# Performance work log

Measured on AMD Instinct MI355X. Metric: run time of the kernel, lower is better.

Reference implementation:

```python
import jax, jax.numpy as jnp
import numpy as np

N, NF1, NF2, NH, OUT, K = 16384, 2000, 10000, 512, 16, 19
BN_EPS = 1e-5

def _bn(x, g, b, m, v):
    # eval-mode BatchNorm1d with running stats
    return (x - m) * jax.lax.rsqrt(v + BN_EPS) * g + b


def setup_inputs() -> dict:
    key = jax.random.key(0)
    ks = jax.random.split(key, 24)
    f32 = jnp.float32
    def w(k, shape):
        return jax.random.normal(k, shape, f32) * 0.02
    inp = {
        "rna": jax.random.normal(ks[0], (N, NF1), f32),
        "atac": jax.random.normal(ks[1], (N, NF2), f32),
        "index_rna": jnp.arange(N, dtype=jnp.int32),
        "index_atac": jnp.arange(N, dtype=jnp.int32),
        "eps": jax.random.normal(ks[2], (N, OUT), f32),
        # RNA encoder
        "W_r1": w(ks[3], (NH, NF1)), "b_r1": jnp.zeros((NH,), f32),
        "g_r": jnp.ones((NH,), f32), "be_r": jnp.zeros((NH,), f32),
        "m_r": jnp.zeros((NH,), f32), "v_r": jnp.ones((NH,), f32),
        "W_rmu": w(ks[4], (OUT, NH)), "b_rmu": jnp.zeros((OUT,), f32),
        "W_rvar": w(ks[5], (OUT, NH)), "b_rvar": jnp.zeros((OUT,), f32),
        # ATAC encoder
        "W_a1": w(ks[6], (NH, NF2)), "b_a1": jnp.zeros((NH,), f32),
        "g_a": jnp.ones((NH,), f32), "be_a": jnp.zeros((NH,), f32),
        "m_a": jnp.zeros((NH,), f32), "v_a": jnp.ones((NH,), f32),
        "W_amu": w(ks[7], (OUT, NH)), "b_amu": jnp.zeros((OUT,), f32),
        "W_avar": w(ks[8], (OUT, NH)), "b_avar": jnp.zeros((OUT,), f32),
        # decoder
        "W_d1": w(ks[9], (NH, OUT)), "b_d1": jnp.zeros((NH,), f32),
        "g_d": jnp.ones((NH,), f32), "be_d": jnp.zeros((NH,), f32),
        "m_d": jnp.zeros((NH,), f32), "v_d": jnp.ones((NH,), f32),
        "W_d4": w(ks[10], (NF1 + NF2, NH)), "b_d4": jnp.zeros((NF1 + NF2,), f32),
        "cluster": jax.random.normal(ks[11], (K, OUT), f32),
    }
    return inp


def reference(rna, atac, index_rna, index_atac, eps,
              W_r1, b_r1, g_r, be_r, m_r, v_r, W_rmu, b_rmu, W_rvar, b_rvar,
              W_a1, b_a1, g_a, be_a, m_a, v_a, W_amu, b_amu, W_avar, b_avar,
              W_d1, b_d1, g_d, be_d, m_d, v_d, W_d4, b_d4, cluster):
    n = rna.shape[0]
    # encoders (dropout is identity in eval mode)
    h_rna = jax.nn.relu(_bn(rna @ W_r1.T + b_r1, g_r, be_r, m_r, v_r))
    zm_rna = h_rna @ W_rmu.T + b_rmu
    zv_rna = jnp.exp(h_rna @ W_rvar.T + b_rvar)
    h_atac = jax.nn.relu(_bn(atac @ W_a1.T + b_a1, g_a, be_a, m_a, v_a))
    zm_atac = h_atac @ W_amu.T + b_amu
    zv_atac = jnp.exp(h_atac @ W_avar.T + b_avar)
    # vectorized scatter replacing the per-sample Python loop
    mu = jnp.ones((n, 2, OUT), rna.dtype)
    var = jnp.ones((n, 2, OUT), rna.dtype)
    mask = jnp.zeros((n, 2, OUT), rna.dtype)
    mu = mu.at[index_rna, 0].set(zm_rna).at[index_atac, 1].set(zm_atac)
    var = var.at[index_rna, 0].set(zv_rna).at[index_atac, 1].set(zv_atac)
    mask = mask.at[index_rna, 0].set(1.0).at[index_atac, 1].set(1.0)
    # product of experts over the modality axis (axis=1)
    T = mask / var
    T_sum = T.sum(axis=1) + 1.0            # [n, OUT]
    z_mu = (mu * T).sum(axis=1) / T_sum
    z_var = 1.0 / T_sum
    # Normal(z_mu, scale=z_var).rsample() with externally supplied eps
    z = z_mu + z_var * eps
    # student-t style soft assignment to clusters
    d2 = jnp.sum((z[:, None, :] - cluster[None, :, :]) ** 2, axis=2)  # [n, K]
    q = 1.0 / (1.0 + d2)
    q = q / q.sum(axis=1, keepdims=True)
    # decoder
    h = jax.nn.relu(_bn(z @ W_d1.T + b_d1, g_d, be_d, m_d, v_d))
    recon_x = h @ W_d4.T + b_d4
    return (recon_x, z_mu, z_var, z, q)
```

## Files before the change

kernel.cpp:

```cpp
#include <hip/hip_runtime.h>

#define NS   16384
#define NF1c 2000
#define NF2c 10000
#define NH   512
#define KC   19
#define NREC 12000

typedef short bf16x8 __attribute__((ext_vector_type(8)));
typedef float f32x4  __attribute__((ext_vector_type(4)));

__device__ __forceinline__ unsigned short f2bf(float x) {
    unsigned int u = __builtin_bit_cast(unsigned int, x);
    u += 0x7FFFu + ((u >> 16) & 1u);
    return (unsigned short)(u >> 16);
}
__device__ __forceinline__ float bf2f(unsigned short h) {
    return __builtin_bit_cast(float, (unsigned int)h << 16);
}

__device__ __forceinline__ void sync_nodrain() {
    asm volatile("s_waitcnt lgkmcnt(0)" ::: "memory");
    __builtin_amdgcn_s_barrier();
    asm volatile("" ::: "memory");
}

__global__ void k_cvt(const float* __restrict__ s, unsigned short* __restrict__ d, int n4) {
    int i = blockIdx.x * blockDim.x + threadIdx.x;
    int st = gridDim.x * blockDim.x;
    for (; i < n4; i += st) {
        float4 f = ((const float4*)s)[i];
        ushort4 o;
        o.x = f2bf(f.x); o.y = f2bf(f.y); o.z = f2bf(f.z); o.w = f2bf(f.w);
        ((ushort4*)d)[i] = o;
    }
}

__global__ void k_prep_st(const float* __restrict__ g, const float* __restrict__ be,
                          const float* __restrict__ m, const float* __restrict__ v,
                          const float* __restrict__ b1,
                          float* __restrict__ s, float* __restrict__ t, int n) {
    int i = blockIdx.x * blockDim.x + threadIdx.x;
    if (i < n) {
        float sc = g[i] * rsqrtf(v[i] + 1e-5f);
        s[i] = sc;
        t[i] = be[i] + (b1[i] - m[i]) * sc;
    }
}

__global__ void k_zero(float* __restrict__ p, int n) {
    int i = blockIdx.x * blockDim.x + threadIdx.x;
    if (i < n) p[i] = 0.f;
}

template<int BK> __device__ __forceinline__ int swz(int r) {
    return (BK == 32) ? ((r >> 1) & 3) : (r & 7);
}

template<int EPI, int A_BF16, int BK>
__global__ __launch_bounds__(256)
void k_gemm(const void* __restrict__ Aptr, const unsigned short* __restrict__ B,
            int K, int Nn, int ntn,
            const float* __restrict__ sc, const float* __restrict__ sh,
            unsigned short* __restrict__ Hout, float* __restrict__ Fout)
{
    constexpr int CH = BK / 8;
    constexpr int JC = CH / 2;
    __shared__ __align__(16) unsigned short As[2][128 * BK];
    __shared__ __align__(16) unsigned short Bs[2][128 * BK];

    const int nwg = gridDim.x;
    const int q8  = nwg >> 3;
    const int L   = (blockIdx.x & 7) * q8 + (blockIdx.x >> 3);
    const int tn  = L % ntn, tm = L / ntn;

    const int tid  = threadIdx.x;
    const int wave = tid >> 6, lane = tid & 63;
    const int wr   = wave >> 1, wc = wave & 1;
    const int lo   = lane & 15, hi = lane >> 4;
    const int srow = tid >> 1, shalf = tid & 1;
    const long arow = (long)tm * 128 + srow;
    const int  brow = tn * 128 + srow;
    const bool bok  = (brow < Nn);

    const float*          Af  = (const float*)Aptr + arow * (long)K;
    const unsigned short* A16 = (const unsigned short*)Aptr + arow * (long)K;
    const unsigned short* Bp  = B + (long)brow * K;

    f32x4 acc[4][4];
#pragma unroll
    for (int i = 0; i < 4; i++)
#pragma unroll
        for (int j = 0; j < 4; j++) acc[i][j] = (f32x4){0.f, 0.f, 0.f, 0.f};

    float4 rfa[BK / 8];
    uint4  ra[JC];
    uint4  rb[JC];

    auto issue_load = [&](int k0, bool tail) {
        const int kb = k0 + shalf * (BK / 2);
        if (A_BF16) {
            if (!tail) {
#pragma unroll
                for (int j = 0; j < JC; j++) ra[j] = *(const uint4*)(A16 + kb + j * 8);
            } else {
#pragma unroll
                for (int j = 0; j < JC; j++) {
                    __align__(16) unsigned short t8[8];
#pragma unroll
                    for (int e = 0; e < 8; e++)
                        t8[e] = (kb + j * 8 + e < K) ? A16[kb + j * 8 + e] : (unsigned short)0;
                    ra[j] = *(uint4*)t8;
                }
            }
        } else {
            if (!tail) {
#pragma unroll
                for (int q = 0; q < BK / 8; q++) rfa[q] = *(const float4*)(Af + kb + q * 4);
            } else {
#pragma unroll
                for (int q = 0; q < BK / 8; q++) {
                    float4 f;
                    f.x = (kb + q * 4 + 0 < K) ? Af[kb + q * 4 + 0] : 0.f;
                    f.y = (kb + q * 4 + 1 < K) ? Af[kb + q * 4 + 1] : 0.f;
                    f.z = (kb + q * 4 + 2 < K) ? Af[kb + q * 4 + 2] : 0.f;
                    f.w = (kb + q * 4 + 3 < K) ? Af[kb + q * 4 + 3] : 0.f;
                    rfa[q] = f;
                }
            }
        }
#pragma unroll
        for (int j = 0; j < JC; j++) rb[j] = (uint4){0, 0, 0, 0};
        if (bok) {
            if (!tail) {
#pragma unroll
                for (int j = 0; j < JC; j++) rb[j] = *(const uint4*)(Bp + kb + j * 8);
            } else {
#pragma unroll
                for (int j = 0; j < JC; j++) {
                    __align__(16) unsigned short t8[8];
#pragma unroll
                    for (int e = 0; e < 8; e++)
                        t8[e] = (kb + j * 8 + e < K) ? Bp[kb + j * 8 + e] : (unsigned short)0;
                    rb[j] = *(uint4*)t8;
                }
            }
        }
    };

    auto write_lds = [&](int buf) {
        char* Ap = (char*)As[buf];
        char* Bq = (char*)Bs[buf];
        const int rbase = srow * (2 * BK);
        const int sw = swz<BK>(srow);
#pragma unroll
        for (int j = 0; j < JC; j++) {
            const int c = shalf * JC + j;
            const int pos = rbase + ((c ^ sw) << 4);
            uint4 av;
            if (A_BF16) {
                av = ra[j];
            } else {
                __align__(16) unsigned short u8[8];
#pragma unroll
                for (int e = 0; e < 8; e++) u8[e] = f2bf(((const float*)&rfa[2 * j])[e]);
                av = *(uint4*)u8;
            }
            *(uint4*)(Ap + pos) = av;
            *(uint4*)(Bq + pos) = rb[j];
        }
    };

    auto compute = [&](int buf) {
        const char* Ap = (const char*)As[buf];
        const char* Bq = (const char*)Bs[buf];
#pragma unroll
        for (int s = 0; s < BK / 32; s++) {
            bf16x8 af[4], bfv[4];
#pragma unroll
            for (int f = 0; f < 4; f++) {
                const int ar = wr * 64 + f * 16 + lo;
                af[f]  = *(const bf16x8*)(Ap + ar * (2 * BK) + (((s * 4 + hi) ^ swz<BK>(ar)) << 4));
                const int br = wc * 64 + f * 16 + lo;
                bfv[f] = *(const bf16x8*)(Bq + br * (2 * BK) + (((s * 4 + hi) ^ swz<BK>(br)) << 4));
            }
#pragma unroll
            for (int i = 0; i < 4; i++)
#pragma unroll
                for (int j = 0; j < 4; j++)
                    acc[i][j] = __builtin_amdgcn_mfma_f32_16x16x32_bf16(af[i], bfv[j], acc[i][j], 0, 0, 0);
        }
    };

    const int ntf = K / BK;
    const bool has_rem = (K % BK) != 0;
    const int nt = ntf + (has_rem ? 1 : 0);
    issue_load(0, has_rem && nt == 1);
    for (int t = 0; t < nt; ++t) {
        write_lds(t & 1);
        if (t + 1 < nt) issue_load((t + 1) * BK, has_rem && (t + 1 == nt - 1));
        sync_nodrain();
        compute(t & 1);
    }

#pragma unroll
    for (int i = 0; i < 4; i++) {
#pragma unroll
        for (int j = 0; j < 4; j++) {
            const int col = tn * 128 + wc * 64 + j * 16 + lo;
#pragma unroll
            for (int r = 0; r < 4; r++) {
                const long row = (long)tm * 128 + wr * 64 + i * 16 + hi * 4 + r;
                float v = acc[i][j][r];
                if (EPI == 0) {
                    v = fmaxf(v * sc[col] + sh[col], 0.f);
                    Hout[row * NH + col] = f2bf(v);
                } else {
                    if (col < Nn) Fout[row * (long)Nn + col] = v + sc[col];
                }
            }
        }
    }
}

__global__ __launch_bounds__(256)
void k_proj(const unsigned short* __restrict__ h_rna,
            const unsigned short* __restrict__ h_atac,
            const float* __restrict__ W_rmu, const float* __restrict__ b_rmu,
            const float* __restrict__ W_rvar, const float* __restrict__ b_rvar,
            const float* __restrict__ W_amu, const float* __restrict__ b_amu,
            const float* __restrict__ W_avar, const float* __restrict__ b_avar,
            const int* __restrict__ idx_rna, const int* __restrict__ idx_atac,
            float* __restrict__ mu0, float* __restrict__ var0,
            float* __restrict__ mu1, float* __restrict__ var1,
            float* __restrict__ mflag)
{
    __shared__ __align__(16) unsigned short hsh[4][2][NH];
    const int wave = threadIdx.x >> 6, lane = threadIdx.x & 63;
    const long i = (long)blockIdx.x * 4 + wave;
    *(uint4*)&hsh[wave][0][lane * 8] = *(const uint4*)(h_rna  + i * NH + lane * 8);
    *(uint4*)&hsh[wave][1][lane * 8] = *(const uint4*)(h_atac + i * NH + lane * 8);
    __syncthreads();
    const int mod = lane >> 5, oo = lane & 31;
    const int isv = oo >> 4, o = oo & 15;
    const float *W, *bias;
    if (mod == 0) { W = isv ? W_rvar : W_rmu; bias = isv ? b_rvar : b_rmu; }
    else          { W = isv ? W_avar : W_amu; bias = isv ? b_avar : b_amu; }
    const unsigned short* hr = hsh[wave][mod];
    const float* wrow = W + o * NH;
    float a = 0.f;
#pragma unroll 4
    for (int k = 0; k < NH; k += 4) {
        float4 w = *(const float4*)(wrow + k);
        a += bf2f(hr[k]) * w.x + bf2f(hr[k+1]) * w.y + bf2f(hr[k+2]) * w.z + bf2f(hr[k+3]) * w.w;
    }
    a += bias[o];
    const int tgt = (mod == 0) ? idx_rna[i] : idx_atac[i];
    float* mu  = mod ? mu1  : mu0;
    float* var = mod ? var1 : var0;
    if (!isv) mu[(long)tgt * 16 + o] = a;
    else      var[(long)tgt * 16 + o] = expf(a);
    if (oo == 0) mflag[(long)mod * NS + tgt] = 1.f;
}

__global__ __launch_bounds__(256)
void k_combine(const float* __restrict__ mu0, const float* __restrict__ var0,
               const float* __restrict__ mu1, const float* __restrict__ var1,
               const float* __restrict__ mflag,
               const float* __restrict__ eps, const float* __restrict__ cluster,
               const float* __restrict__ W_d1,
               const float* __restrict__ s_d, const float* __restrict__ t_d,
               float* __restrict__ o_zmu, float* __restrict__ o_zvar,
               float* __restrict__ o_z, float* __restrict__ o_q,
               unsigned short* __restrict__ h_d)
{
    __shared__ float zsh[4][16];
    const int wave = threadIdx.x >> 6, lane = threadIdx.x & 63;
    const long i = (long)blockIdx.x * 4 + wave;
    if (lane < 16) {
        const int d = lane;
        const float f0 = mflag[i], f1 = mflag[NS + i];
        float ts = 1.f, num = 0.f;
        if (f0 != 0.f) { float iv = 1.f / var0[i*16+d]; ts += iv; num += mu0[i*16+d] * iv; }
        if (f1 != 0.f) { float iv = 1.f / var1[i*16+d]; ts += iv; num += mu1[i*16+d] * iv; }
        const float zm = num / ts, zv = 1.f / ts;
        const float z = zm + zv * eps[i*16+d];
        o_zmu[i*16+d] = zm; o_zvar[i*16+d] = zv; o_z[i*16+d] = z;
        zsh[wave][d] = z;
    }
    __syncthreads();
    float zreg[16];
#pragma unroll
    for (int d = 0; d < 16; d++) zreg[d] = zsh[wave][d];
    float qk = 0.f;
    if (lane < KC) {
        float d2 = 0.f;
#pragma unroll
        for (int d = 0; d < 16; d++) { float df = zreg[d] - cluster[lane*16+d]; d2 += df*df; }
        qk = 1.f / (1.f + d2);
    }
    float ssum = qk;
#pragma unroll
    for (int off = 16; off > 0; off >>= 1) ssum += __shfl_xor(ssum, off, 32);
    if (lane < KC) o_q[i * KC + lane] = qk / ssum;
#pragma unroll
    for (int j = 0; j < 8; j++) {
        const int c = lane + 64 * j;
        float a = 0.f;
#pragma unroll
        for (int d = 0; d < 16; d += 4) {
            float4 w = *(const float4*)(W_d1 + c * 16 + d);
            a += zreg[d] * w.x + zreg[d+1] * w.y + zreg[d+2] * w.z + zreg[d+3] * w.w;
        }
        a = fmaxf(a * s_d[c] + t_d[c], 0.f);
        h_d[i * NH + c] = f2bf(a);
    }
}

extern "C" void kernel_launch(void* const* d_in, const int* in_sizes, int n_in,
                              void* d_out, int out_size, void* d_ws, size_t ws_size,
                              hipStream_t stream)
{
    const float* rna    = (const float*)d_in[0];
    const float* atac   = (const float*)d_in[1];
    const int*   i_rna  = (const int*)d_in[2];
    const int*   i_atac = (const int*)d_in[3];
    const float* eps    = (const float*)d_in[4];
    const float* W_r1   = (const float*)d_in[5];
    const float* b_r1   = (const float*)d_in[6];
    const float* g_r    = (const float*)d_in[7];
    const float* be_r   = (const float*)d_in[8];
    const float* m_r    = (const float*)d_in[9];
    const float* v_r    = (const float*)d_in[10];
    const float* W_rmu  = (const float*)d_in[11];
    const float* b_rmu  = (const float*)d_in[12];
    const float* W_rvar = (const float*)d_in[13];
    const float* b_rvar = (const float*)d_in[14];
    const float* W_a1   = (const float*)d_in[15];
    const float* b_a1   = (const float*)d_in[16];
    const float* g_a    = (const float*)d_in[17];
    const float* be_a   = (const float*)d_in[18];
    const float* m_a    = (const float*)d_in[19];
    const float* v_a    = (const float*)d_in[20];
    const float* W_amu  = (const float*)d_in[21];
    const float* b_amu  = (const float*)d_in[22];
    const float* W_avar = (const float*)d_in[23];
    const float* b_avar = (const float*)d_in[24];
    const float* W_d1   = (const float*)d_in[25];
    const float* b_d1   = (const float*)d_in[26];
    const float* g_d    = (const float*)d_in[27];
    const float* be_d   = (const float*)d_in[28];
    const float* m_d    = (const float*)d_in[29];
    const float* v_d    = (const float*)d_in[30];
    const float* W_d4   = (const float*)d_in[31];
    const float* b_d4   = (const float*)d_in[32];
    const float* clus   = (const float*)d_in[33];
    (void)in_sizes; (void)n_in; (void)out_size;

    char* w = (char*)d_ws;
    size_t off = 0;
    auto carve = [&](size_t bytes) { void* p = w + off; off += (bytes + 255) & ~(size_t)255; return p; };
    unsigned short* wr1b  = (unsigned short*)carve((size_t)NH * NF1c * 2);
    unsigned short* wa1b  = (unsigned short*)carve((size_t)NH * NF2c * 2);
    unsigned short* wd4b  = (unsigned short*)carve((size_t)NREC * NH * 2);
    unsigned short* hrna  = (unsigned short*)carve((size_t)NS * NH * 2);
    unsigned short* hatac = (unsigned short*)carve((size_t)NS * NH * 2);
    unsigned short* hd    = (unsigned short*)carve((size_t)NS * NH * 2);
    float* mu0   = (float*)carve((size_t)NS * 16 * 4);
    float* var0  = (float*)carve((size_t)NS * 16 * 4);
    float* mu1   = (float*)carve((size_t)NS * 16 * 4);
    float* var1  = (float*)carve((size_t)NS * 16 * 4);
    float* mflag = (float*)carve((size_t)2 * NS * 4);
    float* st    = (float*)carve((size_t)6 * NH * 4);
    if (off > ws_size) return;

    float* s_r = st;          float* t_r = st + NH;
    float* s_a = st + 2*NH;   float* t_a = st + 3*NH;
    float* s_d = st + 4*NH;   float* t_d = st + 5*NH;

    float* out    = (float*)d_out;
    float* o_rec  = out;
    float* o_zmu  = out + (size_t)NS * NREC;
    float* o_zvar = o_zmu + (size_t)NS * 16;
    float* o_z    = o_zvar + (size_t)NS * 16;
    float* o_q    = o_z + (size_t)NS * 16;

    k_cvt<<<1024, 256, 0, stream>>>(W_r1, wr1b, NH * NF1c / 4);
    k_cvt<<<2048, 256, 0, stream>>>(W_a1, wa1b, NH * NF2c / 4);
    k_cvt<<<2048, 256, 0, stream>>>(W_d4, wd4b, NREC * NH / 4);
    k_prep_st<<<2, 256, 0, stream>>>(g_r, be_r, m_r, v_r, b_r1, s_r, t_r, NH);
    k_prep_st<<<2, 256, 0, stream>>>(g_a, be_a, m_a, v_a, b_a1, s_a, t_a, NH);
    k_prep_st<<<2, 256, 0, stream>>>(g_d, be_d, m_d, v_d, b_d1, s_d, t_d, NH);
    k_zero<<<(2 * NS + 255) / 256, 256, 0, stream>>>(mflag, 2 * NS);

    dim3 blk(256);
    k_gemm<0, 0, 64><<<512, blk, 0, stream>>>(rna,  wr1b, NF1c, NH, 4, s_r, t_r, hrna,  nullptr);
    k_gemm<0, 0, 64><<<512, blk, 0, stream>>>(atac, wa1b, NF2c, NH, 4, s_a, t_a, hatac, nullptr);
    k_proj<<<NS / 4, blk, 0, stream>>>(hrna, hatac, W_rmu, b_rmu, W_rvar, b_rvar,
                                       W_amu, b_amu, W_avar, b_avar, i_rna, i_atac,
                                       mu0, var0, mu1, var1, mflag);
    k_combine<<<NS / 4, blk, 0, stream>>>(mu0, var0, mu1, var1, mflag, eps, clus,
                                          W_d1, s_d, t_d, o_zmu, o_zvar, o_z, o_q, hd);
    k_gemm<1, 1, 32><<<94 * 128, blk, 0, stream>>>(hd, wd4b, NH, NREC, 94, b_d4, nullptr, nullptr, o_rec);
}
```

Measured before the change: 1.227 ms.

## Deepen GEMM global-load prefetch to two register stages with occupancy hint

The GEMM main loop now keeps two register staging buffers, so global loads for tile t+2 are issued while tile t is written to LDS and computed. This hides more global-memory latency. The loop is unrolled by two, with a tail for odd tile counts. The kernel also gets a launch_bounds minimum of 2 blocks per CU, and float-to-bf16 conversion now uses the hip_bfloat16 constructor with packed 32-bit writes. The extra staging registers may raise register pressure, which conflicts with the two-block occupancy target and could cause spills.

After: 1.294 ms. 5.5% more time.

```diff
diff --git a/kernel.cpp b/kernel.cpp
--- a/kernel.cpp
+++ b/kernel.cpp
@@ -1,4 +1,5 @@
 #include <hip/hip_runtime.h>
+#include <hip/hip_bf16.h>
 
 #define NS   16384
 #define NF1c 2000
@@ -11,9 +12,7 @@
 typedef float f32x4  __attribute__((ext_vector_type(4)));
 
 __device__ __forceinline__ unsigned short f2bf(float x) {
-    unsigned int u = __builtin_bit_cast(unsigned int, x);
-    u += 0x7FFFu + ((u >> 16) & 1u);
-    return (unsigned short)(u >> 16);
+    return __builtin_bit_cast(unsigned short, __hip_bfloat16(x));
 }
 __device__ __forceinline__ float bf2f(unsigned short h) {
     return __builtin_bit_cast(float, (unsigned int)h << 16);
@@ -58,14 +57,13 @@
 }
 
 template<int EPI, int A_BF16, int BK>
-__global__ __launch_bounds__(256)
+__global__ __launch_bounds__(256, 2)
 void k_gemm(const void* __restrict__ Aptr, const unsigned short* __restrict__ B,
             int K, int Nn, int ntn,
             const float* __restrict__ sc, const float* __restrict__ sh,
             unsigned short* __restrict__ Hout, float* __restrict__ Fout)
 {
-    constexpr int CH = BK / 8;
-    constexpr int JC = CH / 2;
+    constexpr int JC = BK / 16;
     __shared__ __align__(16) unsigned short As[2][128 * BK];
     __shared__ __align__(16) unsigned short Bs[2][128 * BK];
 
@@ -93,16 +91,19 @@
 #pragma unroll
         for (int j = 0; j < 4; j++) acc[i][j] = (f32x4){0.f, 0.f, 0.f, 0.f};
 
-    float4 rfa[BK / 8];
-    uint4  ra[JC];
-    uint4  rb[JC];
-
-    auto issue_load = [&](int k0, bool tail) {
+    struct Stage {
+        float4 af[BK / 8];
+        uint4  ah[JC];
+        uint4  b[JC];
+    };
+    Stage s0, s1;
+
+    auto issue = [&](Stage& S, int k0, bool tail) {
         const int kb = k0 + shalf * (BK / 2);
         if (A_BF16) {
             if (!tail) {
 #pragma unroll
-                for (int j = 0; j < JC; j++) ra[j] = *(const uint4*)(A16 + kb + j * 8);
+                for (int j = 0; j < JC; j++) S.ah[j] = *(const uint4*)(A16 + kb + j * 8);
             } else {
 #pragma unroll
                 for (int j = 0; j < JC; j++) {
@@ -110,13 +111,13 @@
 #pragma unroll
                     for (int e = 0; e < 8; e++)
                         t8[e] = (kb + j * 8 + e < K) ? A16[kb + j * 8 + e] : (unsigned short)0;
-                    ra[j] = *(uint4*)t8;
+                    S.ah[j] = *(uint4*)t8;
                 }
             }
         } else {
             if (!tail) {
 #pragma unroll
-                for (int q = 0; q < BK / 8; q++) rfa[q] = *(const float4*)(Af + kb + q * 4);
+                for (int q = 0; q < BK / 8; q++) S.af[q] = *(const float4*)(Af + kb + q * 4);
             } else {
 #pragma unroll
                 for (int q = 0; q < BK / 8; q++) {
@@ -125,16 +126,16 @@
                     f.y = (kb + q * 4 + 1 < K) ? Af[kb + q * 4 + 1] : 0.f;
                     f.z = (kb + q * 4 + 2 < K) ? Af[kb + q * 4 + 2] : 0.f;
                     f.w = (kb + q * 4 + 3 < K) ? Af[kb + q * 4 + 3] : 0.f;
-                    rfa[q] = f;
+                    S.af[q] = f;
                 }
             }
         }
 #pragma unroll
-        for (int j = 0; j < JC; j++) rb[j] = (uint4){0, 0, 0, 0};
+        for (int j = 0; j < JC; j++) S.b[j] = (uint4){0, 0, 0, 0};
         if (bok) {
             if (!tail) {
 #pragma unroll
-                for (int j = 0; j < JC; j++) rb[j] = *(const uint4*)(Bp + kb + j * 8);
+                for (int j = 0; j < JC; j++) S.b[j] = *(const uint4*)(Bp + kb + j * 8);
             } else {
 #pragma unroll
                 for (int j = 0; j < JC; j++) {
@@ -142,13 +143,13 @@
 #pragma unroll
                     for (int e = 0; e < 8; e++)
                         t8[e] = (kb + j * 8 + e < K) ? Bp[kb + j * 8 + e] : (unsigned short)0;
-                    rb[j] = *(uint4*)t8;
+                    S.b[j] = *(uint4*)t8;
                 }
             }
         }
     };
 
-    auto write_lds = [&](int buf) {
+    auto write = [&](int buf, Stage& S) {
         char* Ap = (char*)As[buf];
         char* Bq = (char*)Bs[buf];
         const int rbase = srow * (2 * BK);
@@ -159,19 +160,23 @@
             const int pos = rbase + ((c ^ sw) << 4);
             uint4 av;
             if (A_BF16) {
-                av = ra[j];
+                av = S.ah[j];
             } else {
-                __align__(16) unsigned short u8[8];
-#pragma unroll
-                for (int e = 0; e < 8; e++) u8[e] = f2bf(((const float*)&rfa[2 * j])[e]);
-                av = *(uint4*)u8;
+                unsigned int* w32 = (unsigned int*)&av;
+#pragma unroll
+                for (int e = 0; e < 4; e++) {
+                    const float* fp = (const float*)&S.af[2 * j];
+                    unsigned int lo16 = f2bf(fp[2 * e]);
+                    unsigned int hi16 = f2bf(fp[2 * e + 1]);
+                    w32[e] = lo16 | (hi16 << 16);
+                }
             }
             *(uint4*)(Ap + pos) = av;
-            *(uint4*)(Bq + pos) = rb[j];
+            *(uint4*)(Bq + pos) = S.b[j];
         }
     };
 
-    auto compute = [&](int buf) {
+    auto comp = [&](int buf) {
         const char* Ap = (const char*)As[buf];
         const char* Bq = (const char*)Bs[buf];
 #pragma unroll
@@ -193,14 +198,26 @@
     };
 
     const int ntf = K / BK;
-    const bool has_rem = (K % BK) != 0;
-    const int nt = ntf + (has_rem ? 1 : 0);
-    issue_load(0, has_rem && nt == 1);
-    for (int t = 0; t < nt; ++t) {
-        write_lds(t & 1);
-        if (t + 1 < nt) issue_load((t + 1) * BK, has_rem && (t + 1 == nt - 1));
+    const bool rem = (K % BK) != 0;
+    const int nt = ntf + (rem ? 1 : 0);
+
+    issue(s0, 0, rem && nt == 1);
+    if (nt > 1) issue(s1, BK, rem && nt == 2);
+    int t = 0;
+    for (; t + 2 <= nt; t += 2) {
+        write(0, s0);
+        if (t + 2 < nt) issue(s0, (t + 2) * BK, rem && (t + 2 == nt - 1));
         sync_nodrain();
-        compute(t & 1);
+        comp(0);
+        write(1, s1);
+        if (t + 3 < nt) issue(s1, (t + 3) * BK, rem && (t + 3 == nt - 1));
+        sync_nodrain();
+        comp(1);
+    }
+    if (t < nt) {
+        write(0, s0);
+        sync_nodrain();
+        comp(0);
     }
 
 #pragma unroll
```

## Retile encoder GEMMs to 128x64 tiles with BK=32 and raise occupancy

Applied to the files above, without the earlier changes.

The GEMM template now fixes BK at 32 and takes the N tile width as a parameter. The encoder GEMMs use 128x64 tiles over twice as many workgroups, and launch bounds request 4 waves per SIMD. MFMA issue is wrapped in s_setprio, and float-to-bf16 conversion switches to the HIP intrinsic with packed writes. The aim is more resident workgroups, so the streaming fp32 activation loads get better latency hiding. In exchange, B tiles are re-read across more workgroups and each LDS stage carries a smaller K slice.

Result: slower. 1.751 ms (+42.8%).

```diff
diff --git a/kernel.cpp b/kernel.cpp
--- a/kernel.cpp
+++ b/kernel.cpp
@@ -1,4 +1,5 @@
 #include <hip/hip_runtime.h>
+#include <hip/hip_bf16.h>
 
 #define NS   16384
 #define NF1c 2000
@@ -11,9 +12,7 @@
 typedef float f32x4  __attribute__((ext_vector_type(4)));
 
 __device__ __forceinline__ unsigned short f2bf(float x) {
-    unsigned int u = __builtin_bit_cast(unsigned int, x);
-    u += 0x7FFFu + ((u >> 16) & 1u);
-    return (unsigned short)(u >> 16);
+    return __builtin_bit_cast(unsigned short, __hip_bfloat16(x));
 }
 __device__ __forceinline__ float bf2f(unsigned short h) {
     return __builtin_bit_cast(float, (unsigned int)h << 16);
@@ -53,21 +52,18 @@
     if (i < n) p[i] = 0.f;
 }
 
-template<int BK> __device__ __forceinline__ int swz(int r) {
-    return (BK == 32) ? ((r >> 1) & 3) : (r & 7);
-}
-
-template<int EPI, int A_BF16, int BK>
-__global__ __launch_bounds__(256)
+__device__ __forceinline__ int swz(int r) { return (r >> 1) & 3; }
+
+template<int EPI, int A_BF16, int BN>
+__global__ __launch_bounds__(256, 4)
 void k_gemm(const void* __restrict__ Aptr, const unsigned short* __restrict__ B,
             int K, int Nn, int ntn,
             const float* __restrict__ sc, const float* __restrict__ sh,
             unsigned short* __restrict__ Hout, float* __restrict__ Fout)
 {
-    constexpr int CH = BK / 8;
-    constexpr int JC = CH / 2;
-    __shared__ __align__(16) unsigned short As[2][128 * BK];
-    __shared__ __align__(16) unsigned short Bs[2][128 * BK];
+    constexpr int NB = BN / 32;
+    __shared__ __align__(16) unsigned short As[2][128 * 32];
+    __shared__ __align__(16) unsigned short Bs[2][BN * 32];
 
     const int nwg = gridDim.x;
     const int q8  = nwg >> 3;
@@ -78,136 +74,154 @@
     const int wave = tid >> 6, lane = tid & 63;
     const int wr   = wave >> 1, wc = wave & 1;
     const int lo   = lane & 15, hi = lane >> 4;
-    const int srow = tid >> 1, shalf = tid & 1;
-    const long arow = (long)tm * 128 + srow;
-    const int  brow = tn * 128 + srow;
+
+    const int srowA = tid >> 1, shalfA = tid & 1;
+    const int srowB  = (BN == 128) ? (tid >> 1) : (tid >> 2);
+    const int schB   = (BN == 128) ? ((tid & 1) * 2) : (tid & 3);
+    constexpr int BCH = (BN == 128) ? 2 : 1;
+
+    const long arow = (long)tm * 128 + srowA;
+    const int  brow = tn * BN + srowB;
     const bool bok  = (brow < Nn);
 
     const float*          Af  = (const float*)Aptr + arow * (long)K;
     const unsigned short* A16 = (const unsigned short*)Aptr + arow * (long)K;
     const unsigned short* Bp  = B + (long)brow * K;
 
-    f32x4 acc[4][4];
+    f32x4 acc[4][NB];
 #pragma unroll
     for (int i = 0; i < 4; i++)
 #pragma unroll
-        for (int j = 0; j < 4; j++) acc[i][j] = (f32x4){0.f, 0.f, 0.f, 0.f};
-
-    float4 rfa[BK / 8];
-    uint4  ra[JC];
-    uint4  rb[JC];
-
-    auto issue_load = [&](int k0, bool tail) {
-        const int kb = k0 + shalf * (BK / 2);
+        for (int j = 0; j < NB; j++) acc[i][j] = (f32x4){0.f, 0.f, 0.f, 0.f};
+
+    float4 rfa[4];
+    uint4  rah[2];
+    uint4  rb[BCH];
+
+    auto issue = [&](int k0, bool tail) {
+        const int kbA = k0 + shalfA * 16;
         if (A_BF16) {
             if (!tail) {
 #pragma unroll
-                for (int j = 0; j < JC; j++) ra[j] = *(const uint4*)(A16 + kb + j * 8);
+                for (int j = 0; j < 2; j++) rah[j] = *(const uint4*)(A16 + kbA + j * 8);
             } else {
 #pragma unroll
-                for (int j = 0; j < JC; j++) {
+                for (int j = 0; j < 2; j++) {
                     __align__(16) unsigned short t8[8];
 #pragma unroll
                     for (int e = 0; e < 8; e++)
-                        t8[e] = (kb + j * 8 + e < K) ? A16[kb + j * 8 + e] : (unsigned short)0;
-                    ra[j] = *(uint4*)t8;
+                        t8[e] = (kbA + j * 8 + e < K) ? A16[kbA + j * 8 + e] : (unsigned short)0;
+                    rah[j] = *(uint4*)t8;
                 }
             }
         } else {
             if (!tail) {
 #pragma unroll
-                for (int q = 0; q < BK / 8; q++) rfa[q] = *(const float4*)(Af + kb + q * 4);
+                for (int q = 0; q < 4; q++) rfa[q] = *(const float4*)(Af + kbA + q * 4);
             } else {
 #pragma unroll
-                for (int q = 0; q < BK / 8; q++) {
+                for (int q = 0; q < 4; q++) {
                     float4 f;
-                    f.x = (kb + q * 4 + 0 < K) ? Af[kb + q * 4 + 0] : 0.f;
-                    f.y = (kb + q * 4 + 1 < K) ? Af[kb + q * 4 + 1] : 0.f;
-                    f.z = (kb + q * 4 + 2 < K) ? Af[kb + q * 4 + 2] : 0.f;
-                    f.w = (kb + q * 4 + 3 < K) ? Af[kb + q * 4 + 3] : 0.f;
+                    f.x = (kbA + q * 4 + 0 < K) ? Af[kbA + q * 4 + 0] : 0.f;
+                    f.y = (kbA + q * 4 + 1 < K) ? Af[kbA + q * 4 + 1] : 0.f;
+                    f.z = (kbA + q * 4 + 2 < K) ? Af[kbA + q * 4 + 2] : 0.f;
+                    f.w = (kbA + q * 4 + 3 < K) ? Af[kbA + q * 4 + 3] : 0.f;
                     rfa[q] = f;
                 }
             }
         }
 #pragma unroll
-        for (int j = 0; j < JC; j++) rb[j] = (uint4){0, 0, 0, 0};
+        for (int j = 0; j < BCH; j++) rb[j] = (uint4){0, 0, 0, 0};
         if (bok) {
             if (!tail) {
 #pragma unroll
-                for (int j = 0; j < JC; j++) rb[j] = *(const uint4*)(Bp + kb + j * 8);
+                for (int j = 0; j < BCH; j++)
+                    rb[j] = *(const uint4*)(Bp + k0 + (schB + j) * 8);
             } else {
 #pragma unroll
-                for (int j = 0; j < JC; j++) {
+                for (int j = 0; j < BCH; j++) {
                     __align__(16) unsigned short t8[8];
 #pragma unroll
-                    for (int e = 0; e < 8; e++)
-                        t8[e] = (kb + j * 8 + e < K) ? Bp[kb + j * 8 + e] : (unsigned short)0;
+                    for (int e = 0; e < 8; e++) {
+                        const int kk = k0 + (schB + j) * 8 + e;
+                        t8[e] = (kk < K) ? Bp[kk] : (unsigned short)0;
+                    }
                     rb[j] = *(uint4*)t8;
                 }
             }
         }
     };
 
-    auto write_lds = [&](int buf) {
+    auto write = [&](int buf) {
         char* Ap = (char*)As[buf];
         char* Bq = (char*)Bs[buf];
-        const int rbase = srow * (2 * BK);
-        const int sw = swz<BK>(srow);
-#pragma unroll
-        for (int j = 0; j < JC; j++) {
-            const int c = shalf * JC + j;
-            const int pos = rbase + ((c ^ sw) << 4);
+        const int rbaseA = srowA * 64;
+        const int swA = swz(srowA);
+#pragma unroll
+        for (int j = 0; j < 2; j++) {
+            const int c = shalfA * 2 + j;
             uint4 av;
             if (A_BF16) {
-                av = ra[j];
+                av = rah[j];
             } else {
-                __align__(16) unsigned short u8[8];
-#pragma unroll
-                for (int e = 0; e < 8; e++) u8[e] = f2bf(((const float*)&rfa[2 * j])[e]);
-                av = *(uint4*)u8;
+                unsigned int* w32 = (unsigned int*)&av;
+                const float* fp = (const float*)&rfa[2 * j];
+#pragma unroll
+                for (int e = 0; e < 4; e++) {
+                    unsigned int l16 = f2bf(fp[2 * e]);
+                    unsigned int h16 = f2bf(fp[2 * e + 1]);
+                    w32[e] = l16 | (h16 << 16);
+                }
             }
-            *(uint4*)(Ap + pos) = av;
-            *(uint4*)(Bq + pos) = rb[j];
-        }
+            *(uint4*)(Ap + rbaseA + ((c ^ swA) << 4)) = av;
+        }
+        const int rbaseB = srowB * 64;
+        const int swB = swz(srowB);
+#pragma unroll
+        for (int j = 0; j < BCH; j++)
+            *(uint4*)(Bq + rbaseB + (((schB + j) ^ swB) << 4)) = rb[j];
     };
 
-    auto compute = [&](int buf) {
+    auto comp = [&](int buf) {
         const char* Ap = (const char*)As[buf];
         const char* Bq = (const char*)Bs[buf];
-#pragma unroll
-        for (int s = 0; s < BK / 32; s++) {
-            bf16x8 af[4], bfv[4];
-#pragma unroll
-            for (int f = 0; f < 4; f++) {
-                const int ar = wr * 64 + f * 16 + lo;
-                af[f]  = *(const bf16x8*)(Ap + ar * (2 * BK) + (((s * 4 + hi) ^ swz<BK>(ar)) << 4));
-                const int br = wc * 64 + f * 16 + lo;
-                bfv[f] = *(const bf16x8*)(Bq + br * (2 * BK) + (((s * 4 + hi) ^ swz<BK>(br)) << 4));
-            }
-#pragma unroll
-            for (int i = 0; i < 4; i++)
-#pragma unroll
-                for (int j = 0; j < 4; j++)
-                    acc[i][j] = __builtin_amdgcn_mfma_f32_16x16x32_bf16(af[i], bfv[j], acc[i][j], 0, 0, 0);
-        }
+        bf16x8 af[4], bfv[NB];
+#pragma unroll
+        for (int f = 0; f < 4; f++) {
+            const int ar = wr * 64 + f * 16 + lo;
+            af[f] = *(const bf16x8*)(Ap + ar * 64 + ((hi ^ swz(ar)) << 4));
+        }
+#pragma unroll
+        for (int f = 0; f < NB; f++) {
+            const int br = wc * (BN / 2) + f * 16 + lo;
+            bfv[f] = *(const bf16x8*)(Bq + br * 64 + ((hi ^ swz(br)) << 4));
+        }
+        __builtin_amdgcn_s_setprio(1);
+#pragma unroll
+        for (int i = 0; i < 4; i++)
+#pragma unroll
+            for (int j = 0; j < NB; j++)
+                acc[i][j] = __builtin_amdgcn_mfma_f32_16x16x32_bf16(af[i], bfv[j], acc[i][j], 0, 0, 0);
+        __builtin_amdgcn_s_setprio(0);
     };
 
-    const int ntf = K / BK;
-    const bool has_rem = (K % BK) != 0;
-    const int nt = ntf + (has_rem ? 1 : 0);
-    issue_load(0, has_rem && nt == 1);
+    const int ntf = K / 32;
+    const bool rem = (K % 32) != 0;
+    const int nt = ntf + (rem ? 1 : 0);
+
+    issue(0, rem && nt == 1);
     for (int t = 0; t < nt; ++t) {
-        write_lds(t & 1);
-        if (t + 1 < nt) issue_load((t + 1) * BK, has_rem && (t + 1 == nt - 1));
+        write(t & 1);
+        if (t + 1 < nt) issue((t + 1) * 32, rem && (t + 1 == nt - 1));
         sync_nodrain();
-        compute(t & 1);
+        comp(t & 1);
     }
 
 #pragma unroll
     for (int i = 0; i < 4; i++) {
 #pragma unroll
-        for (int j = 0; j < 4; j++) {
-            const int col = tn * 128 + wc * 64 + j * 16 + lo;
+        for (int j = 0; j < NB; j++) {
+            const int col = tn * BN + wc * (BN / 2) + j * 16 + lo;
 #pragma unroll
             for (int r = 0; r < 4; r++) {
                 const long row = (long)tm * 128 + wr * 64 + i * 16 + hi * 4 + r;
@@ -394,12 +408,12 @@
     k_zero<<<(2 * NS + 255) / 256, 256, 0, stream>>>(mflag, 2 * NS);
 
     dim3 blk(256);
-    k_gemm<0, 0, 64><<<512, blk, 0, stream>>>(rna,  wr1b, NF1c, NH, 4, s_r, t_r, hrna,  nullptr);
-    k_gemm<0, 0, 64><<<512, blk, 0, stream>>>(atac, wa1b, NF2c, NH, 4, s_a, t_a, hatac, nullptr);
+    k_gemm<0, 0, 64><<<1024, blk, 0, stream>>>(rna,  wr1b, NF1c, NH, 8, s_r, t_r, hrna,  nullptr);
+    k_gemm<0, 0, 64><<<1024, blk, 0, stream>>>(atac, wa1b, NF2c, NH, 8, s_a, t_a, hatac, nullptr);
     k_proj<<<NS / 4, blk, 0, stream>>>(hrna, hatac, W_rmu, b_rmu, W_rvar, b_rvar,
                                        W_amu, b_amu, W_avar, b_avar, i_rna, i_atac,
                                        mu0, var0, mu1, var1, mflag);
     k_combine<<<NS / 4, blk, 0, stream>>>(mu0, var0, mu1, var1, mflag, eps, clus,
                                           W_d1, s_d, t_d, o_zmu, o_zvar, o_z, o_q, hd);
-    k_gemm<1, 1, 32><<<94 * 128, blk, 0, stream>>>(hd, wd4b, NH, NREC, 94, b_d4, nullptr, nullptr, o_rec);
-}
+    k_gemm<1, 1, 128><<<94 * 128, blk, 0, stream>>>(hd, wd4b, NH, NREC, 94, b_d4, nullptr, nullptr, o_rec);
+}
```

## Add dedicated decoder GEMM using direct global-to-LDS loads with padded weights

Applied to the files above, without the earlier changes.

Replaces the templated bf16 decoder GEMM with a dedicated kernel that loads tiles straight from global memory into LDS via global_load_lds, using a pre-swizzled source address. W_d4 is converted into a zero-padded buffer so that no bounds checks are needed on B loads. MFMA blocks run under raised s_setprio. The change also swaps the manual f32-to-bf16 rounding for the HIP bfloat16 conversion and packs pairs into 32-bit words. The decoder GEMM writes about 786MB of fp32 output, so the store path probably still dominates and the load-path gains may be small.

Result: no change. 1.225 ms (-0.2%).

```diff
diff --git a/kernel.cpp b/kernel.cpp
--- a/kernel.cpp
+++ b/kernel.cpp
@@ -1,19 +1,19 @@
 #include <hip/hip_runtime.h>
-
-#define NS   16384
-#define NF1c 2000
-#define NF2c 10000
-#define NH   512
-#define KC   19
-#define NREC 12000
+#include <hip/hip_bf16.h>
+
+#define NS    16384
+#define NF1c  2000
+#define NF2c  10000
+#define NH    512
+#define KC    19
+#define NREC  12000
+#define NRECP 12032
 
 typedef short bf16x8 __attribute__((ext_vector_type(8)));
 typedef float f32x4  __attribute__((ext_vector_type(4)));
 
 __device__ __forceinline__ unsigned short f2bf(float x) {
-    unsigned int u = __builtin_bit_cast(unsigned int, x);
-    u += 0x7FFFu + ((u >> 16) & 1u);
-    return (unsigned short)(u >> 16);
+    return __builtin_bit_cast(unsigned short, __hip_bfloat16(x));
 }
 __device__ __forceinline__ float bf2f(unsigned short h) {
     return __builtin_bit_cast(float, (unsigned int)h << 16);
@@ -23,6 +23,16 @@
     asm volatile("s_waitcnt lgkmcnt(0)" ::: "memory");
     __builtin_amdgcn_s_barrier();
     asm volatile("" ::: "memory");
+}
+
+template<int BK> __device__ __forceinline__ int swz(int r) {
+    return (BK == 32) ? ((r >> 1) & 3) : (r & 7);
+}
+
+__device__ __forceinline__ void gload16(const unsigned short* g, unsigned short* l) {
+    __builtin_amdgcn_global_load_lds(
+        (const __attribute__((address_space(1))) void*)g,
+        (__attribute__((address_space(3))) void*)l, 16, 0, 0);
 }
 
 __global__ void k_cvt(const float* __restrict__ s, unsigned short* __restrict__ d, int n4) {
@@ -33,6 +43,26 @@
         ushort4 o;
         o.x = f2bf(f.x); o.y = f2bf(f.y); o.z = f2bf(f.z); o.w = f2bf(f.w);
         ((ushort4*)d)[i] = o;
+    }
+}
+
+__global__ void k_cvt_pad(const float* __restrict__ s, unsigned short* __restrict__ d,
+                          int K, int Rv, long nchunks) {
+    long i = (long)blockIdx.x * blockDim.x + threadIdx.x;
+    const long stp = (long)gridDim.x * blockDim.x;
+    const int Kp8 = K / 8;
+    for (; i < nchunks; i += stp) {
+        const long row = i / Kp8;
+        const int  col = (int)(i - row * Kp8) * 8;
+        __align__(16) unsigned short u[8] = {0, 0, 0, 0, 0, 0, 0, 0};
+        if (row < Rv) {
+            const float* p = s + row * (long)K + col;
+            float4 f0 = *(const float4*)p;
+            float4 f1 = *(const float4*)(p + 4);
+            u[0] = f2bf(f0.x); u[1] = f2bf(f0.y); u[2] = f2bf(f0.z); u[3] = f2bf(f0.w);
+            u[4] = f2bf(f1.x); u[5] = f2bf(f1.y); u[6] = f2bf(f1.z); u[7] = f2bf(f1.w);
+        }
+        *(uint4*)(d + row * (long)K + col) = *(uint4*)u;
     }
 }
 
@@ -53,19 +83,14 @@
     if (i < n) p[i] = 0.f;
 }
 
-template<int BK> __device__ __forceinline__ int swz(int r) {
-    return (BK == 32) ? ((r >> 1) & 3) : (r & 7);
-}
-
-template<int EPI, int A_BF16, int BK>
 __global__ __launch_bounds__(256)
 void k_gemm(const void* __restrict__ Aptr, const unsigned short* __restrict__ B,
             int K, int Nn, int ntn,
             const float* __restrict__ sc, const float* __restrict__ sh,
-            unsigned short* __restrict__ Hout, float* __restrict__ Fout)
+            unsigned short* __restrict__ Hout)
 {
-    constexpr int CH = BK / 8;
-    constexpr int JC = CH / 2;
+    constexpr int BK = 64;
+    constexpr int JC = BK / 16;
     __shared__ __align__(16) unsigned short As[2][128 * BK];
     __shared__ __align__(16) unsigned short Bs[2][128 * BK];
 
@@ -83,9 +108,8 @@
     const int  brow = tn * 128 + srow;
     const bool bok  = (brow < Nn);
 
-    const float*          Af  = (const float*)Aptr + arow * (long)K;
-    const unsigned short* A16 = (const unsigned short*)Aptr + arow * (long)K;
-    const unsigned short* Bp  = B + (long)brow * K;
+    const float*          Af = (const float*)Aptr + arow * (long)K;
+    const unsigned short* Bp = B + (long)brow * K;
 
     f32x4 acc[4][4];
 #pragma unroll
@@ -94,39 +118,22 @@
         for (int j = 0; j < 4; j++) acc[i][j] = (f32x4){0.f, 0.f, 0.f, 0.f};
 
     float4 rfa[BK / 8];
-    uint4  ra[JC];
     uint4  rb[JC];
 
-    auto issue_load = [&](int k0, bool tail) {
+    auto issue = [&](int k0, bool tail) {
         const int kb = k0 + shalf * (BK / 2);
-        if (A_BF16) {
-            if (!tail) {
-#pragma unroll
-                for (int j = 0; j < JC; j++) ra[j] = *(const uint4*)(A16 + kb + j * 8);
-            } else {
-#pragma unroll
-                for (int j = 0; j < JC; j++) {
-                    __align__(16) unsigned short t8[8];
-#pragma unroll
-                    for (int e = 0; e < 8; e++)
-                        t8[e] = (kb + j * 8 + e < K) ? A16[kb + j * 8 + e] : (unsigned short)0;
-                    ra[j] = *(uint4*)t8;
-                }
-            }
+        if (!tail) {
+#pragma unroll
+            for (int q = 0; q < BK / 8; q++) rfa[q] = *(const float4*)(Af + kb + q * 4);
         } else {
-            if (!tail) {
-#pragma unroll
-                for (int q = 0; q < BK / 8; q++) rfa[q] = *(const float4*)(Af + kb + q * 4);
-            } else {
-#pragma unroll
-                for (int q = 0; q < BK / 8; q++) {
-                    float4 f;
-                    f.x = (kb + q * 4 + 0 < K) ? Af[kb + q * 4 + 0] : 0.f;
-                    f.y = (kb + q * 4 + 1 < K) ? Af[kb + q * 4 + 1] : 0.f;
-                    f.z = (kb + q * 4 + 2 < K) ? Af[kb + q * 4 + 2] : 0.f;
-                    f.w = (kb + q * 4 + 3 < K) ? Af[kb + q * 4 + 3] : 0.f;
-                    rfa[q] = f;
-                }
+#pragma unroll
+            for (int q = 0; q < BK / 8; q++) {
+                float4 f;
+                f.x = (kb + q * 4 + 0 < K) ? Af[kb + q * 4 + 0] : 0.f;
+                f.y = (kb + q * 4 + 1 < K) ? Af[kb + q * 4 + 1] : 0.f;
+                f.z = (kb + q * 4 + 2 < K) ? Af[kb + q * 4 + 2] : 0.f;
+                f.w = (kb + q * 4 + 3 < K) ? Af[kb + q * 4 + 3] : 0.f;
+                rfa[q] = f;
             }
         }
 #pragma unroll
@@ -148,7 +155,7 @@
         }
     };
 
-    auto write_lds = [&](int buf) {
+    auto write = [&](int buf) {
         char* Ap = (char*)As[buf];
         char* Bq = (char*)Bs[buf];
         const int rbase = srow * (2 * BK);
@@ -158,20 +165,20 @@
             const int c = shalf * JC + j;
             const int pos = rbase + ((c ^ sw) << 4);
             uint4 av;
-            if (A_BF16) {
-                av = ra[j];
-            } else {
-                __align__(16) unsigned short u8[8];
-#pragma unroll
-                for (int e = 0; e < 8; e++) u8[e] = f2bf(((const float*)&rfa[2 * j])[e]);
-                av = *(uint4*)u8;
+            unsigned int* w32 = (unsigned int*)&av;
+            const float* fp = (const float*)&rfa[2 * j];
+#pragma unroll
+            for (int e = 0; e < 4; e++) {
+                unsigned int l16 = f2bf(fp[2 * e]);
+                unsigned int h16 = f2bf(fp[2 * e + 1]);
+                w32[e] = l16 | (h16 << 16);
             }
             *(uint4*)(Ap + pos) = av;
             *(uint4*)(Bq + pos) = rb[j];
         }
     };
 
-    auto compute = [&](int buf) {
+    auto comp = [&](int buf) {
         const char* Ap = (const char*)As[buf];
         const char* Bq = (const char*)Bs[buf];
 #pragma unroll
@@ -193,14 +200,14 @@
     };
 
     const int ntf = K / BK;
-    const bool has_rem = (K % BK) != 0;
-    const int nt = ntf + (has_rem ? 1 : 0);
-    issue_load(0, has_rem && nt == 1);
+    const bool rem = (K % BK) != 0;
+    const int nt = ntf + (rem ? 1 : 0);
+    issue(0, rem && nt == 1);
     for (int t = 0; t < nt; ++t) {
-        write_lds(t & 1);
-        if (t + 1 < nt) issue_load((t + 1) * BK, has_rem && (t + 1 == nt - 1));
+        write(t & 1);
+        if (t + 1 < nt) issue((t + 1) * BK, rem && (t + 1 == nt - 1));
         sync_nodrain();
-        compute(t & 1);
+        comp(t & 1);
     }
 
 #pragma unroll
@@ -211,13 +218,97 @@
 #pragma unroll
             for (int r = 0; r < 4; r++) {
                 const long row = (long)tm * 128 + wr * 64 + i * 16 + hi * 4 + r;
-                float v = acc[i][j][r];
-                if (EPI == 0) {
-                    v = fmaxf(v * sc[col] + sh[col], 0.f);
-                    Hout[row * NH + col] = f2bf(v);
-                } else {
-                    if (col < Nn) Fout[row * (long)Nn + col] = v + sc[col];
-                }
+                float v = fmaxf(acc[i][j][r] * sc[col] + sh[col], 0.f);
+                Hout[row * NH + col] = f2bf(v);
+            }
+        }
+    }
+}
+
+__global__ __launch_bounds__(256)
+void k_rec(const unsigned short* __restrict__ A, const unsigned short* __restrict__ B,
+           const float* __restrict__ bias, float* __restrict__ Fout)
+{
+    __shared__ __align__(16) unsigned short As[2][128 * 32];
+    __shared__ __align__(16) unsigned short Bs[2][128 * 32];
+
+    const int q8 = gridDim.x >> 3;
+    const int L  = (blockIdx.x & 7) * q8 + (blockIdx.x >> 3);
+    const int tn = L % 94, tm = L / 94;
+
+    const int tid  = threadIdx.x;
+    const int wave = tid >> 6, lane = tid & 63;
+    const int wr = wave >> 1, wc = wave & 1;
+    const int lo = lane & 15, hi = lane >> 4;
+
+    const int rloc = lane >> 2, cch = lane & 3;
+    const int row0 = wave * 32 + rloc;
+    const int row1 = wave * 32 + 16 + rloc;
+    const unsigned short* Ad0 = A + (long)(tm * 128 + row0) * NH + (cch ^ swz<32>(row0)) * 8;
+    const unsigned short* Ad1 = A + (long)(tm * 128 + row1) * NH + (cch ^ swz<32>(row1)) * 8;
+    const unsigned short* Bd0 = B + (long)(tn * 128 + row0) * NH + (cch ^ swz<32>(row0)) * 8;
+    const unsigned short* Bd1 = B + (long)(tn * 128 + row1) * NH + (cch ^ swz<32>(row1)) * 8;
+
+    f32x4 acc[4][4];
+#pragma unroll
+    for (int i = 0; i < 4; i++)
+#pragma unroll
+        for (int j = 0; j < 4; j++) acc[i][j] = (f32x4){0.f, 0.f, 0.f, 0.f};
+
+    auto issue = [&](int buf) {
+        gload16(Ad0, &As[buf][wave * 1024]);
+        gload16(Ad1, &As[buf][wave * 1024 + 512]);
+        gload16(Bd0, &Bs[buf][wave * 1024]);
+        gload16(Bd1, &Bs[buf][wave * 1024 + 512]);
+        Ad0 += 32; Ad1 += 32; Bd0 += 32; Bd1 += 32;
+    };
+    auto comp = [&](int buf) {
+        const char* Ap = (const char*)As[buf];
+        const char* Bq = (const char*)Bs[buf];
+        bf16x8 af[4], bfv[4];
+#pragma unroll
+        for (int f = 0; f < 4; f++) {
+            const int ar = wr * 64 + f * 16 + lo;
+            af[f] = *(const bf16x8*)(Ap + ar * 64 + ((hi ^ swz<32>(ar)) << 4));
+            const int br = wc * 64 + f * 16 + lo;
+            bfv[f] = *(const bf16x8*)(Bq + br * 64 + ((hi ^ swz<32>(br)) << 4));
+        }
+        __builtin_amdgcn_s_setprio(1);
+#pragma unroll
+        for (int i = 0; i < 4; i++)
+#pragma unroll
+            for (int j = 0; j < 4; j++)
+                acc[i][j] = __builtin_amdgcn_mfma_f32_16x16x32_bf16(af[i], bfv[j], acc[i][j], 0, 0, 0);
+        __builtin_amdgcn_s_setprio(0);
+    };
+
+    const int nt = NH / 32;
+    issue(0);
+    asm volatile("s_waitcnt vmcnt(0)" ::: "memory");
+    __builtin_amdgcn_s_barrier();
+    asm volatile("" ::: "memory");
+
+    for (int t = 0; t < nt; ++t) {
+        const int c = t & 1;
+        const bool more = (t + 1 < nt);
+        if (more) issue(c ^ 1);
+        comp(c);
+        if (more) {
+            asm volatile("s_waitcnt vmcnt(0) lgkmcnt(0)" ::: "memory");
+            __builtin_amdgcn_s_barrier();
+            asm volatile("" ::: "memory");
+        }
+    }
+
+#pragma unroll
+    for (int i = 0; i < 4; i++) {
+#pragma unroll
+        for (int j = 0; j < 4; j++) {
+            const int col = tn * 128 + wc * 64 + j * 16 + lo;
+#pragma unroll
+            for (int r = 0; r < 4; r++) {
+                const long row = (long)tm * 128 + wr * 64 + i * 16 + hi * 4 + r;
+                if (col < NREC) Fout[row * (long)NREC + col] = acc[i][j][r] + bias[col];
             }
         }
     }
@@ -362,7 +453,7 @@
     auto carve = [&](size_t bytes) { void* p = w + off; off += (bytes + 255) & ~(size_t)255; return p; };
     unsigned short* wr1b  = (unsigned short*)carve((size_t)NH * NF1c * 2);
     unsigned short* wa1b  = (unsigned short*)carve((size_t)NH * NF2c * 2);
-    unsigned short* wd4b  = (unsigned short*)carve((size_t)NREC * NH * 2);
+    unsigned short* wd4b  = (unsigned short*)carve((size_t)NRECP * NH * 2);
     unsigned short* hrna  = (unsigned short*)carve((size_t)NS * NH * 2);
     unsigned short* hatac = (unsigned short*)carve((size_t)NS * NH * 2);
     unsigned short* hd    = (unsigned short*)carve((size_t)NS * NH * 2);
@@ -387,19 +478,19 @@
 
     k_cvt<<<1024, 256, 0, stream>>>(W_r1, wr1b, NH * NF1c / 4);
     k_cvt<<<2048, 256, 0, stream>>>(W_a1, wa1b, NH * NF2c / 4);
-    k_cvt<<<2048, 256, 0, stream>>>(W_d4, wd4b, NREC * NH / 4);
+    k_cvt_pad<<<2048, 256, 0, stream>>>(W_d4, wd4b, NH, NREC, (long)NRECP * (NH / 8));
     k_prep_st<<<2, 256, 0, stream>>>(g_r, be_r, m_r, v_r, b_r1, s_r, t_r, NH);
     k_prep_st<<<2, 256, 0, stream>>>(g_a, be_a, m_a, v_a, b_a1, s_a, t_a, NH);
     k_prep_st<<<2, 256, 0, stream>>>(g_d, be_d, m_d, v_d, b_d1, s_d, t_d, NH);
     k_zero<<<(2 * NS + 255) / 256, 256, 0, stream>>>(mflag, 2 * NS);
 
     dim3 blk(256);
-    k_gemm<0, 0, 64><<<512, blk, 0, stream>>>(rna,  wr1b, NF1c, NH, 4, s_r, t_r, hrna,  nullptr);
-    k_gemm<0, 0, 64><<<512, blk, 0, stream>>>(atac, wa1b, NF2c, NH, 4, s_a, t_a, hatac, nullptr);
+    k_gemm<<<512, blk, 0, stream>>>(rna,  wr1b, NF1c, NH, 4, s_r, t_r, hrna);
+    k_gemm<<<512, blk, 0, stream>>>(atac, wa1b, NF2c, NH, 4, s_a, t_a, hatac);
     k_proj<<<NS / 4, blk, 0, stream>>>(hrna, hatac, W_rmu, b_rmu, W_rvar, b_rvar,
                                        W_amu, b_amu, W_avar, b_avar, i_rna, i_atac,
                                        mu0, var0, mu1, var1, mflag);
     k_combine<<<NS / 4, blk, 0, stream>>>(mu0, var0, mu1, var1, mflag, eps, clus,
                                           W_d1, s_d, t_d, o_zmu, o_zvar, o_z, o_q, hd);
-    k_gemm<1, 1, 32><<<94 * 128, blk, 0, stream>>>(hd, wd4b, NH, NREC, 94, b_d4, nullptr, nullptr, o_rec);
-}
+    k_rec<<<94 * 128, blk, 0, stream>>>(hd, wd4b, b_d4, o_rec);
+}
```
